# Optimization experiments

Hardware: AMD Instinct MI355X
Metric: run time of the kernel (lower is better)

The kernel has to match this reference:

```python
import jax, jax.numpy as jnp
import numpy as np
import math

B, L, H, E = 4, 2048, 16, 64
S, D = L, E


def setup_inputs() -> dict:
    key = jax.random.key(0)
    kq, kk, kv = jax.random.split(key, 3)
    queries = jax.random.normal(kq, (B, L, H, E), dtype=jnp.float32)
    keys = jax.random.normal(kk, (B, S, H, E), dtype=jnp.float32)
    values = jax.random.normal(kv, (B, S, H, D), dtype=jnp.float32)
    # TriangularCausalMask: True above the diagonal => masked out
    attn_mask = jnp.broadcast_to(
        jnp.triu(jnp.ones((L, S), dtype=bool), k=1)[None, None], (B, 1, L, S)
    )
    return {"queries": queries, "keys": keys, "values": values, "attn_mask": attn_mask}


def reference(queries, keys, values, attn_mask):
    Edim = queries.shape[-1]
    scale = 1.0 / math.sqrt(Edim)  # self.scale is None -> 1/sqrt(E)
    # scores: [B, H, L, S]
    scores = jnp.einsum("blhe,bshe->bhls", queries, keys)
    # mask BEFORE scaling (as in original); -inf is invariant under positive scale
    scores = jnp.where(attn_mask, -jnp.inf, scores)
    attn = jax.nn.softmax(scale * scores, axis=-1)  # dropout p=0.0 -> identity
    out = jnp.einsum("bhls,bshd->blhd", attn, values)
    return out
```

## Files before the change

### kernel.cpp

```cpp
#include <hip/hip_runtime.h>


#define B_ 4
#define L_ 2048
#define H_ 16

typedef __attribute__((ext_vector_type(4))) float f32x4;
typedef __attribute__((ext_vector_type(8))) short bf16x8;

#if __has_builtin(__builtin_amdgcn_exp2f)
#define EXP2(x) __builtin_amdgcn_exp2f(x)
#else
#define EXP2(x) exp2f(x)
#endif

#if __has_builtin(__builtin_amdgcn_sched_barrier)
#define SCHED_FENCE() __builtin_amdgcn_sched_barrier(0)
#else
#define SCHED_FENCE()
#endif

__device__ __forceinline__ unsigned pkbf(float lo, float hi) {
    union { float f; unsigned u; } a, b;
    a.f = lo; b.f = hi;
    return __builtin_amdgcn_perm(b.u, a.u, 0x07060302u);
}

__global__ __launch_bounds__(256, 2) void attn_fwd(
    const float* __restrict__ Q, const float* __restrict__ K,
    const float* __restrict__ V, float* __restrict__ O)
{
    __shared__ unsigned smem[13312];
    unsigned* Pl = smem + 9216;

    const int tid = threadIdx.x;
    const int w   = tid >> 6;
    const int l   = tid & 63;
    const int l15 = l & 15;
    const int qd  = l >> 4;
    const int bh  = blockIdx.x & 63;
    const int pr  = blockIdx.x >> 6;
    const int b   = bh >> 4, h = bh & 15;
    const float cexp = 0.125f * 1.44269504088896340736f;

    const float* Kb = K + (((size_t)b * L_) * H_ + h) * 64;
    const float* Vb = V + (((size_t)b * L_) * H_ + h) * 64;
    unsigned* Pw = Pl + w * 1024;

    const int krow = tid >> 2, kq = tid & 3;
    const int vsp  = tid >> 3, vdg = tid & 7;
    const int vswz = vsp ^ (4 * vdg);
    const int grpr = l ^ (4 * ((l >> 4) & 1));

    for (int ph = 0; ph < 2; ++ph) {
        const int t    = ph ? pr : 15 - pr;
        const int qr0  = t * 128 + w * 32;
        const int mykb = (qr0 >> 6) + 1;
        const int nkb  = 2 * (t + 1);

        bf16x8 qf[2][2];
#pragma unroll
        for (int rt = 0; rt < 2; ++rt) {
            const int row = qr0 + 16 * rt + l15;
            const float* qp = Q + (((size_t)b * L_ + row) * H_ + h) * 64 + qd * 8;
#pragma unroll
            for (int ke = 0; ke < 2; ++ke) {
                float4 f0 = *(const float4*)(qp + ke * 32);
                float4 f1 = *(const float4*)(qp + ke * 32 + 4);
                union { unsigned u[4]; bf16x8 v; } cv;
                cv.u[0] = pkbf(f0.x * cexp, f0.y * cexp);
                cv.u[1] = pkbf(f0.z * cexp, f0.w * cexp);
                cv.u[2] = pkbf(f1.x * cexp, f1.y * cexp);
                cv.u[3] = pkbf(f1.z * cexp, f1.w * cexp);
                qf[rt][ke] = cv.v;
            }
        }

        f32x4 o[4][2];
#pragma unroll
        for (int dt = 0; dt < 4; ++dt)
#pragma unroll
            for (int rt = 0; rt < 2; ++rt)
                o[dt][rt] = (f32x4){0.f, 0.f, 0.f, 0.f};
        float ls[2] = {0.f, 0.f};

        {
            const float* kg = Kb + (size_t)krow * 1024 + kq * 16;
            float4 k0 = *(const float4*)(kg + 0);
            float4 k1 = *(const float4*)(kg + 4);
            float4 k2 = *(const float4*)(kg + 8);
            float4 k3 = *(const float4*)(kg + 12);
            const float* vg = Vb + (size_t)(2 * vsp) * 1024 + vdg * 8;
            float4 v0 = *(const float4*)(vg + 0);
            float4 v1 = *(const float4*)(vg + 4);
            float4 v2 = *(const float4*)(vg + 1024);
            float4 v3 = *(const float4*)(vg + 1028);
            unsigned* kd = smem + krow * 36 + kq * 8;
            uint4 w0, w1;
            w0.x = pkbf(k0.x, k0.y); w0.y = pkbf(k0.z, k0.w);
            w0.z = pkbf(k1.x, k1.y); w0.w = pkbf(k1.z, k1.w);
            w1.x = pkbf(k2.x, k2.y); w1.y = pkbf(k2.z, k2.w);
            w1.z = pkbf(k3.x, k3.y); w1.w = pkbf(k3.z, k3.w);
            *(uint4*)kd = w0;
            *(uint4*)(kd + 4) = w1;
            unsigned* vd = smem + 2304 + (8 * vdg) * 36 + vswz;
            vd[0 * 36] = pkbf(v0.x, v2.x);
            vd[1 * 36] = pkbf(v0.y, v2.y);
            vd[2 * 36] = pkbf(v0.z, v2.z);
            vd[3 * 36] = pkbf(v0.w, v2.w);
            vd[4 * 36] = pkbf(v1.x, v3.x);
            vd[5 * 36] = pkbf(v1.y, v3.y);
            vd[6 * 36] = pkbf(v1.z, v3.z);
            vd[7 * 36] = pkbf(v1.w, v3.w);
        }
        __syncthreads();

        for (int kb = 0; kb < nkb; ++kb) {
            const bool more = (kb + 1 < nkb);
            float4 nk0, nk1, nk2, nk3, nv0, nv1, nv2, nv3;
            if (more) {
                const float* kg = Kb + (size_t)((kb + 1) * 64 + krow) * 1024 + kq * 16;
                nk0 = *(const float4*)(kg + 0);
                nk1 = *(const float4*)(kg + 4);
                nk2 = *(const float4*)(kg + 8);
                nk3 = *(const float4*)(kg + 12);
                const float* vg = Vb + (size_t)((kb + 1) * 64 + 2 * vsp) * 1024 + vdg * 8;
                nv0 = *(const float4*)(vg + 0);
                nv1 = *(const float4*)(vg + 4);
                nv2 = *(const float4*)(vg + 1024);
                nv3 = *(const float4*)(vg + 1028);
            }

            if (kb < mykb) {
                const unsigned* Kl = smem + (kb & 1) * 4608;
                const unsigned* Vl = Kl + 2304;

                f32x4 st[4][2];
#pragma unroll
                for (int kt = 0; kt < 4; ++kt)
#pragma unroll
                    for (int rt = 0; rt < 2; ++rt)
                        st[kt][rt] = (f32x4){0.f, 0.f, 0.f, 0.f};
#pragma unroll
                for (int kt = 0; kt < 4; ++kt)
#pragma unroll
                    for (int ke = 0; ke < 2; ++ke) {
                        bf16x8 a = *(const bf16x8*)(Kl + (kt * 16 + l15) * 36 + ke * 16 + qd * 4);
                        st[kt][0] = __builtin_amdgcn_mfma_f32_16x16x32_bf16(a, qf[0][ke], st[kt][0], 0, 0, 0);
                        st[kt][1] = __builtin_amdgcn_mfma_f32_16x16x32_bf16(a, qf[1][ke], st[kt][1], 0, 0, 0);
                    }

                if (kb == mykb - 1) {
#pragma unroll
                    for (int kt = 0; kt < 4; ++kt)
#pragma unroll
                        for (int rt = 0; rt < 2; ++rt) {
                            const int rowg = qr0 + 16 * rt + l15;
#pragma unroll
                            for (int r = 0; r < 4; ++r) {
                                const int key = kb * 64 + kt * 16 + 4 * qd + r;
                                if (key > rowg) st[kt][rt][r] = -1e30f;
                            }
                        }
                }

                float sacc0 = 0.f, sacc1 = 0.f;
#pragma unroll
                for (int kt = 0; kt < 4; ++kt)
#pragma unroll
                    for (int r = 0; r < 4; ++r) {
                        float p0 = EXP2(st[kt][0][r]);
                        float p1 = EXP2(st[kt][1][r]);
                        st[kt][0][r] = p0;
                        st[kt][1][r] = p1;
                        sacc0 += p0;
                        sacc1 += p1;
                    }
                ls[0] += sacc0;
                ls[1] += sacc1;

#pragma unroll
                for (int kt = 0; kt < 4; ++kt)
#pragma unroll
                    for (int rt = 0; rt < 2; ++rt) {
                        uint2 pv;
                        pv.x = pkbf(st[kt][rt][0], st[kt][rt][1]);
                        pv.y = pkbf(st[kt][rt][2], st[kt][rt][3]);
                        const int grp = (32 * (kt & 1) + 16 * (qd >> 1) + l15) ^ (4 * (qd >> 1));
                        *(uint2*)(Pw + (kt >> 1) * 512 + rt * 256 + grp * 4 + 2 * (qd & 1)) = pv;
                    }

                bf16x8 vf[2][4];
#pragma unroll
                for (int se = 0; se < 2; ++se)
#pragma unroll
                    for (int dt = 0; dt < 4; ++dt) {
                        const int col = (se * 16 + qd * 4) ^ (4 * (2 * dt + (l15 >> 3)));
                        vf[se][dt] = *(const bf16x8*)(Vl + (dt * 16 + l15) * 36 + col);
                    }

#pragma unroll
                for (int se = 0; se < 2; ++se)
#pragma unroll
                    for (int rt = 0; rt < 2; ++rt) {
                        bf16x8 pb = *(const bf16x8*)(Pw + se * 512 + rt * 256 + grpr * 4);
#pragma unroll
                        for (int dt = 0; dt < 4; ++dt)
                            o[dt][rt] = __builtin_amdgcn_mfma_f32_16x16x32_bf16(vf[se][dt], pb, o[dt][rt], 0, 0, 0);
                    }
            }

            if (more) {
                SCHED_FENCE();
                unsigned* bK = smem + ((kb + 1) & 1) * 4608;
                unsigned* kd = bK + krow * 36 + kq * 8;
                uint4 w0, w1;
                w0.x = pkbf(nk0.x, nk0.y); w0.y = pkbf(nk0.z, nk0.w);
                w0.z = pkbf(nk1.x, nk1.y); w0.w = pkbf(nk1.z, nk1.w);
                w1.x = pkbf(nk2.x, nk2.y); w1.y = pkbf(nk2.z, nk2.w);
                w1.z = pkbf(nk3.x, nk3.y); w1.w = pkbf(nk3.z, nk3.w);
                *(uint4*)kd = w0;
                *(uint4*)(kd + 4) = w1;
                unsigned* vd = bK + 2304 + (8 * vdg) * 36 + vswz;
                vd[0 * 36] = pkbf(nv0.x, nv2.x);
                vd[1 * 36] = pkbf(nv0.y, nv2.y);
                vd[2 * 36] = pkbf(nv0.z, nv2.z);
                vd[3 * 36] = pkbf(nv0.w, nv2.w);
                vd[4 * 36] = pkbf(nv1.x, nv3.x);
                vd[5 * 36] = pkbf(nv1.y, nv3.y);
                vd[6 * 36] = pkbf(nv1.z, nv3.z);
                vd[7 * 36] = pkbf(nv1.w, nv3.w);
                __syncthreads();
            }
        }

#pragma unroll
        for (int rt = 0; rt < 2; ++rt) {
            float s = ls[rt];
            s += __shfl_xor(s, 16);
            s += __shfl_xor(s, 32);
            const float inv = 1.0f / s;
            const int row = qr0 + 16 * rt + l15;
            float* op = O + (((size_t)b * L_ + row) * H_ + h) * 64 + qd * 4;
#pragma unroll
            for (int dt = 0; dt < 4; ++dt) {
                float4 wv;
                wv.x = o[dt][rt][0] * inv;
                wv.y = o[dt][rt][1] * inv;
                wv.z = o[dt][rt][2] * inv;
                wv.w = o[dt][rt][3] * inv;
                *(float4*)(op + dt * 16) = wv;
            }
        }
        if (ph == 0) __syncthreads();
    }
}

extern "C" void kernel_launch(void* const* d_in, const int* in_sizes, int n_in,
                              void* d_out, int out_size, void* d_ws, size_t ws_size,
                              hipStream_t stream) {
    const float* Q = (const float*)d_in[0];
    const float* K = (const float*)d_in[1];
    const float* V = (const float*)d_in[2];
    float* O = (float*)d_out;

    dim3 grid(64 * 8);
    dim3 block(256);
    hipLaunchKernelGGL(attn_fwd, grid, block, 0, stream, Q, K, V, O);
}
```

Before: 210.2 us.

## Permute K rows in LDS so P stays in registers for PV MFMA

K rows are written to shared memory in a permuted order, so the QK^T MFMA output layout directly matches the B-operand layout the PV MFMA needs. The P matrix is then packed to bf16 in registers instead of going through a per-wave LDS staging buffer. The causal mask key index is remapped to the new order. This removes LDS writes and reads of P and shrinks shared memory, which may allow higher occupancy.

```diff
diff --git a/kernel.cpp b/kernel.cpp
--- a/kernel.cpp
+++ b/kernel.cpp
@@ -30,8 +30,7 @@
     const float* __restrict__ Q, const float* __restrict__ K,
     const float* __restrict__ V, float* __restrict__ O)
 {
-    __shared__ unsigned smem[13312];
-    unsigned* Pl = smem + 9216;
+    __shared__ unsigned smem[9216];
 
     const int tid = threadIdx.x;
     const int w   = tid >> 6;
@@ -45,12 +44,12 @@
 
     const float* Kb = K + (((size_t)b * L_) * H_ + h) * 64;
     const float* Vb = V + (((size_t)b * L_) * H_ + h) * 64;
-    unsigned* Pw = Pl + w * 1024;
 
     const int krow = tid >> 2, kq = tid & 3;
+    const int kmrow = (((krow >> 2) & 1) << 5) | (((krow >> 5) & 1) << 4)
+                    | (((krow >> 3) & 3) << 2) | (krow & 3);
     const int vsp  = tid >> 3, vdg = tid & 7;
     const int vswz = vsp ^ (4 * vdg);
-    const int grpr = l ^ (4 * ((l >> 4) & 1));
 
     for (int ph = 0; ph < 2; ++ph) {
         const int t    = ph ? pr : 15 - pr;
@@ -95,7 +94,7 @@
             float4 v1 = *(const float4*)(vg + 4);
             float4 v2 = *(const float4*)(vg + 1024);
             float4 v3 = *(const float4*)(vg + 1028);
-            unsigned* kd = smem + krow * 36 + kq * 8;
+            unsigned* kd = smem + kmrow * 36 + kq * 8;
             uint4 w0, w1;
             w0.x = pkbf(k0.x, k0.y); w0.y = pkbf(k0.z, k0.w);
             w0.z = pkbf(k1.x, k1.y); w0.w = pkbf(k1.z, k1.w);
@@ -158,7 +157,8 @@
                             const int rowg = qr0 + 16 * rt + l15;
 #pragma unroll
                             for (int r = 0; r < 4; ++r) {
-                                const int key = kb * 64 + kt * 16 + 4 * qd + r;
+                                const int key = kb * 64 + (kt & 1) * 32 + qd * 8
+                                              + (kt >> 1) * 4 + r;
                                 if (key > rowg) st[kt][rt][r] = -1e30f;
                             }
                         }
@@ -179,17 +179,6 @@
                 ls[0] += sacc0;
                 ls[1] += sacc1;
 
-#pragma unroll
-                for (int kt = 0; kt < 4; ++kt)
-#pragma unroll
-                    for (int rt = 0; rt < 2; ++rt) {
-                        uint2 pv;
-                        pv.x = pkbf(st[kt][rt][0], st[kt][rt][1]);
-                        pv.y = pkbf(st[kt][rt][2], st[kt][rt][3]);
-                        const int grp = (32 * (kt & 1) + 16 * (qd >> 1) + l15) ^ (4 * (qd >> 1));
-                        *(uint2*)(Pw + (kt >> 1) * 512 + rt * 256 + grp * 4 + 2 * (qd & 1)) = pv;
-                    }
-
                 bf16x8 vf[2][4];
 #pragma unroll
                 for (int se = 0; se < 2; ++se)
@@ -203,17 +192,21 @@
                 for (int se = 0; se < 2; ++se)
 #pragma unroll
                     for (int rt = 0; rt < 2; ++rt) {
-                        bf16x8 pb = *(const bf16x8*)(Pw + se * 512 + rt * 256 + grpr * 4);
+                        union { unsigned u[4]; bf16x8 v; } pb;
+                        pb.u[0] = pkbf(st[se][rt][0], st[se][rt][1]);
+                        pb.u[1] = pkbf(st[se][rt][2], st[se][rt][3]);
+                        pb.u[2] = pkbf(st[se + 2][rt][0], st[se + 2][rt][1]);
+                        pb.u[3] = pkbf(st[se + 2][rt][2], st[se + 2][rt][3]);
 #pragma unroll
                         for (int dt = 0; dt < 4; ++dt)
-                            o[dt][rt] = __builtin_amdgcn_mfma_f32_16x16x32_bf16(vf[se][dt], pb, o[dt][rt], 0, 0, 0);
+                            o[dt][rt] = __builtin_amdgcn_mfma_f32_16x16x32_bf16(vf[se][dt], pb.v, o[dt][rt], 0, 0, 0);
                     }
             }
 
             if (more) {
                 SCHED_FENCE();
                 unsigned* bK = smem + ((kb + 1) & 1) * 4608;
-                unsigned* kd = bK + krow * 36 + kq * 8;
+                unsigned* kd = bK + kmrow * 36 + kq * 8;
                 uint4 w0, w1;
                 w0.x = pkbf(nk0.x, nk0.y); w0.y = pkbf(nk0.z, nk0.w);
                 w0.z = pkbf(nk1.x, nk1.y); w0.w = pkbf(nk1.z, nk1.w);
```

New measurement: 207.1 us. About the same (-1.4%).
